# Kernel tuning notes

Hardware: AMD Instinct MI355X
Metric: run time of the kernel (lower is better)

The kernel has to match this reference:

```python
import jax, jax.numpy as jnp
import numpy as np

EPS = 1e-5


def _layernorm(x, w, b):
    mu = jnp.mean(x, axis=-1, keepdims=True)
    var = jnp.var(x, axis=-1, keepdims=True)
    return (x - mu) * jax.lax.rsqrt(var + EPS) * w + b


def setup_inputs() -> dict:
    key = jax.random.key(0)
    ks = jax.random.split(key, 5)
    B, I, H = 8192, 1024, 1024
    inp = {
        "input": jax.random.normal(ks[0], (B, I), dtype=jnp.float32),
        "hx": jax.random.normal(ks[1], (B, H), dtype=jnp.float32),
        "cx": jax.random.normal(ks[2], (B, H), dtype=jnp.float32),
        # parameters (torch initializes weights with randn; LN weight=1, bias=0)
        "weight_ih": jax.random.normal(ks[3], (4 * H, I), dtype=jnp.float32),
        "weight_hh": jax.random.normal(ks[4], (4 * H, H), dtype=jnp.float32),
        "ln_i_w": jnp.ones((4 * H,), jnp.float32),
        "ln_i_b": jnp.zeros((4 * H,), jnp.float32),
        "ln_h_w": jnp.ones((4 * H,), jnp.float32),
        "ln_h_b": jnp.zeros((4 * H,), jnp.float32),
        "ln_c_w": jnp.ones((H,), jnp.float32),
        "ln_c_b": jnp.zeros((H,), jnp.float32),
    }
    return inp


def reference(input, hx, cx, weight_ih, weight_hh,
              ln_i_w, ln_i_b, ln_h_w, ln_h_b, ln_c_w, ln_c_b):
    # gate pre-activations: [B, 4H]
    igates = _layernorm(input @ weight_ih.T, ln_i_w, ln_i_b)
    hgates = _layernorm(hx @ weight_hh.T, ln_h_w, ln_h_b)
    gates = igates + hgates
    ingate, forgetgate, cellgate, outgate = jnp.split(gates, 4, axis=-1)
    ingate = jax.nn.sigmoid(ingate)
    forgetgate = jax.nn.sigmoid(forgetgate)
    cellgate = jnp.tanh(cellgate)
    outgate = jax.nn.sigmoid(outgate)
    cy = _layernorm(forgetgate * cx + ingate * cellgate, ln_c_w, ln_c_b)
    hy = outgate * jnp.tanh(cy)  # activation=Tanh, dropout p=0 is identity
    return (hy, cy)
```

## Files before the change

### kernel.cpp

```cpp
#include <hip/hip_runtime.h>
#include <hip/hip_bf16.h>
#include <cstdint>
#include <cstddef>

typedef __bf16 bf16_t;
typedef bf16_t bf16x8 __attribute__((ext_vector_type(8)));
typedef bf16_t bf16x4v __attribute__((ext_vector_type(4)));
typedef float floatx4 __attribute__((ext_vector_type(4)));

static constexpr int B_ = 8192;
static constexpr int H_ = 1024;
static constexpr int G4 = 4096;
static constexpr int K_ = 1024;

__device__ inline void async_copy16(const bf16_t* g, bf16_t* l) {
  auto l3 = (__attribute__((address_space(3))) void*)(uint32_t)(uintptr_t)l;
  __builtin_amdgcn_global_load_lds(
      (__attribute__((address_space(1))) void*)(uintptr_t)g, l3, 16, 0, 0);
}

__global__ __launch_bounds__(256) void cast_f32_to_bf16(
    const float* __restrict__ src, bf16_t* __restrict__ dst, int n4) {
  int i = blockIdx.x * blockDim.x + threadIdx.x;
  if (i < n4) {
    const float4 v = ((const float4*)src)[i];
    bf16x4v o;
    o[0] = (bf16_t)v.x; o[1] = (bf16_t)v.y;
    o[2] = (bf16_t)v.z; o[3] = (bf16_t)v.w;
    ((bf16x4v*)dst)[i] = o;
  }
}

__global__ __launch_bounds__(256) void gemm_bt_dual(
    const bf16_t* __restrict__ A0, const bf16_t* __restrict__ A1,
    const bf16_t* __restrict__ W0, const bf16_t* __restrict__ W1,
    bf16_t* __restrict__ C0, bf16_t* __restrict__ C1) {
  constexpr int N = G4, K = K_;
  const bf16_t* A = blockIdx.z ? A1 : A0;
  const bf16_t* W = blockIdx.z ? W1 : W0;
  bf16_t*       C = blockIdx.z ? C1 : C0;

  __shared__ bf16_t As[128 * 32];
  __shared__ bf16_t Bs[128 * 32];

  const int tid  = threadIdx.x;
  const int lane = tid & 63;
  const int wid  = tid >> 6;
  const int wm   = wid >> 1, wn = wid & 1;
  const int lrow = lane & 15, quad = lane >> 4;

  const int m0 = blockIdx.y * 128;
  const int n0 = blockIdx.x * 128;

  const int L0 = tid;
  const int L1 = 256 + tid;
  const bf16_t* gA0 = A + (size_t)(m0 + (L0 >> 2)) * K + (L0 & 3) * 8;
  const bf16_t* gA1 = A + (size_t)(m0 + (L1 >> 2)) * K + (L1 & 3) * 8;
  const bf16_t* gB0 = W + (size_t)(n0 + (L0 >> 2)) * K + (L0 & 3) * 8;
  const bf16_t* gB1 = W + (size_t)(n0 + (L1 >> 2)) * K + (L1 & 3) * 8;
  bf16_t* lA0 = As + wid * 512;
  bf16_t* lA1 = As + 2048 + wid * 512;
  bf16_t* lB0 = Bs + wid * 512;
  bf16_t* lB1 = Bs + 2048 + wid * 512;

  floatx4 acc[4][4] = {};

  for (int k0 = 0; k0 < K; k0 += 32) {
    __syncthreads();
    async_copy16(gA0 + k0, lA0);
    async_copy16(gA1 + k0, lA1);
    async_copy16(gB0 + k0, lB0);
    async_copy16(gB1 + k0, lB1);
    __syncthreads();

    bf16x8 af[4], bfr[4];
#pragma unroll
    for (int i = 0; i < 4; ++i)
      af[i] = *(const bf16x8*)&As[(wm * 64 + i * 16 + lrow) * 32 + quad * 8];
#pragma unroll
    for (int j = 0; j < 4; ++j)
      bfr[j] = *(const bf16x8*)&Bs[(wn * 64 + j * 16 + lrow) * 32 + quad * 8];
#pragma unroll
    for (int i = 0; i < 4; ++i)
#pragma unroll
      for (int j = 0; j < 4; ++j)
        acc[i][j] = __builtin_amdgcn_mfma_f32_16x16x32_bf16(af[i], bfr[j],
                                                            acc[i][j], 0, 0, 0);
  }

#pragma unroll
  for (int i = 0; i < 4; ++i) {
    const int mbase = m0 + wm * 64 + i * 16 + quad * 4;
#pragma unroll
    for (int j = 0; j < 4; ++j) {
      const int n = n0 + wn * 64 + j * 16 + lrow;
#pragma unroll
      for (int r = 0; r < 4; ++r)
        C[(size_t)(mbase + r) * N + n] = (bf16_t)acc[i][j][r];
    }
  }
}

__device__ inline float sigmoid_f(float x) { return 1.0f / (1.0f + __expf(-x)); }
__device__ inline float tanh_f(float x) {
  float e = __expf(2.0f * x);
  return 1.0f - 2.0f / (e + 1.0f);
}
__device__ inline int swz(int n) { return n + (n >> 4); }

__global__ __launch_bounds__(256) void ln_lstm_epilogue(
    const bf16_t* __restrict__ IG, const bf16_t* __restrict__ HG,
    const float* __restrict__ cx,
    const float* __restrict__ wi, const float* __restrict__ bi,
    const float* __restrict__ wh, const float* __restrict__ bh,
    const float* __restrict__ wc, const float* __restrict__ bc,
    float* __restrict__ hy_out, float* __restrict__ cy_out) {
  const int b = blockIdx.x;
  const int tid = threadIdx.x;
  const int lane = tid & 63;
  const int wid = tid >> 6;

  __shared__ float gates[4096 + 256];
  __shared__ float red[4][4];

  const bf16_t* ig = IG + (size_t)b * 4096;
  const bf16_t* hg = HG + (size_t)b * 4096;

  float vi[16], vh[16];
  {
    bf16x8 a0 = *(const bf16x8*)(ig + tid * 16);
    bf16x8 a1 = *(const bf16x8*)(ig + tid * 16 + 8);
    bf16x8 c0 = *(const bf16x8*)(hg + tid * 16);
    bf16x8 c1 = *(const bf16x8*)(hg + tid * 16 + 8);
#pragma unroll
    for (int e = 0; e < 8; ++e) {
      vi[e] = (float)a0[e]; vi[8 + e] = (float)a1[e];
      vh[e] = (float)c0[e]; vh[8 + e] = (float)c1[e];
    }
  }
  float si = 0, qi = 0, sh = 0, qh = 0;
#pragma unroll
  for (int k = 0; k < 16; ++k) {
    si += vi[k]; qi = fmaf(vi[k], vi[k], qi);
    sh += vh[k]; qh = fmaf(vh[k], vh[k], qh);
  }
#pragma unroll
  for (int off = 32; off; off >>= 1) {
    si += __shfl_down(si, off); qi += __shfl_down(qi, off);
    sh += __shfl_down(sh, off); qh += __shfl_down(qh, off);
  }
  if (lane == 0) { red[wid][0] = si; red[wid][1] = qi; red[wid][2] = sh; red[wid][3] = qh; }
  __syncthreads();
  si = red[0][0] + red[1][0] + red[2][0] + red[3][0];
  qi = red[0][1] + red[1][1] + red[2][1] + red[3][1];
  sh = red[0][2] + red[1][2] + red[2][2] + red[3][2];
  qh = red[0][3] + red[1][3] + red[2][3] + red[3][3];

  const float invN = 1.0f / 4096.0f;
  const float mui = si * invN, muh = sh * invN;
  const float rsi = rsqrtf(fmaxf(qi * invN - mui * mui, 0.0f) + 1e-5f);
  const float rsh = rsqrtf(fmaxf(qh * invN - muh * muh, 0.0f) + 1e-5f);

#pragma unroll
  for (int k4 = 0; k4 < 4; ++k4) {
    const int nb = tid * 16 + k4 * 4;
    const float4 wiv = *(const float4*)(wi + nb);
    const float4 biv = *(const float4*)(bi + nb);
    const float4 whv = *(const float4*)(wh + nb);
    const float4 bhv = *(const float4*)(bh + nb);
    const float wia[4] = {wiv.x, wiv.y, wiv.z, wiv.w};
    const float bia[4] = {biv.x, biv.y, biv.z, biv.w};
    const float wha[4] = {whv.x, whv.y, whv.z, whv.w};
    const float bha[4] = {bhv.x, bhv.y, bhv.z, bhv.w};
#pragma unroll
    for (int j = 0; j < 4; ++j) {
      const int k = k4 * 4 + j;
      const float g = (vi[k] - mui) * rsi * wia[j] + bia[j] +
                      (vh[k] - muh) * rsh * wha[j] + bha[j];
      gates[swz(nb + j)] = g;
    }
  }
  __syncthreads();

  const float4 cx4 = *(const float4*)(cx + (size_t)b * 1024 + tid * 4);
  const float cxa[4] = {cx4.x, cx4.y, cx4.z, cx4.w};
  float cv[4], ov[4];
  float sc = 0, qc = 0;
#pragma unroll
  for (int j = 0; j < 4; ++j) {
    const int h = tid * 4 + j;
    const float in_g = sigmoid_f(gates[swz(h)]);
    const float fo_g = sigmoid_f(gates[swz(h + 1024)]);
    const float ce_g = tanh_f(gates[swz(h + 2048)]);
    ov[j] = sigmoid_f(gates[swz(h + 3072)]);
    const float c = fo_g * cxa[j] + in_g * ce_g;
    cv[j] = c;
    sc += c; qc = fmaf(c, c, qc);
  }
#pragma unroll
  for (int off = 32; off; off >>= 1) {
    sc += __shfl_down(sc, off); qc += __shfl_down(qc, off);
  }
  if (lane == 0) { red[wid][0] = sc; red[wid][1] = qc; }
  __syncthreads();
  sc = red[0][0] + red[1][0] + red[2][0] + red[3][0];
  qc = red[0][1] + red[1][1] + red[2][1] + red[3][1];
  const float invH = 1.0f / 1024.0f;
  const float muc = sc * invH;
  const float rsc = rsqrtf(fmaxf(qc * invH - muc * muc, 0.0f) + 1e-5f);

  const float4 wc4 = ((const float4*)wc)[tid];
  const float4 bc4 = ((const float4*)bc)[tid];
  const float wca[4] = {wc4.x, wc4.y, wc4.z, wc4.w};
  const float bca[4] = {bc4.x, bc4.y, bc4.z, bc4.w};
  float4 hyv, cyv;
  float cya[4], hya[4];
#pragma unroll
  for (int j = 0; j < 4; ++j) {
    const float cyn = (cv[j] - muc) * rsc * wca[j] + bca[j];
    cya[j] = cyn;
    hya[j] = ov[j] * tanh_f(cyn);
  }
  cyv.x = cya[0]; cyv.y = cya[1]; cyv.z = cya[2]; cyv.w = cya[3];
  hyv.x = hya[0]; hyv.y = hya[1]; hyv.z = hya[2]; hyv.w = hya[3];
  *(float4*)(cy_out + (size_t)b * 1024 + tid * 4) = cyv;
  *(float4*)(hy_out + (size_t)b * 1024 + tid * 4) = hyv;
}

extern "C" void kernel_launch(void* const* d_in, const int* in_sizes, int n_in,
                              void* d_out, int out_size, void* d_ws, size_t ws_size,
                              hipStream_t stream) {
  const float* input  = (const float*)d_in[0];
  const float* hx     = (const float*)d_in[1];
  const float* cx     = (const float*)d_in[2];
  const float* w_ih   = (const float*)d_in[3];
  const float* w_hh   = (const float*)d_in[4];
  const float* ln_i_w = (const float*)d_in[5];
  const float* ln_i_b = (const float*)d_in[6];
  const float* ln_h_w = (const float*)d_in[7];
  const float* ln_h_b = (const float*)d_in[8];
  const float* ln_c_w = (const float*)d_in[9];
  const float* ln_c_b = (const float*)d_in[10];

  float* out = (float*)d_out;
  float* hy = out;
  float* cy = out + (size_t)B_ * H_;

  bf16_t* Abf = (bf16_t*)d_ws;
  bf16_t* Hbf = Abf + (size_t)B_ * K_;
  bf16_t* Wib = Hbf + (size_t)B_ * K_;
  bf16_t* Whb = Wib + (size_t)G4 * K_;
  bf16_t* IG  = Whb + (size_t)G4 * K_;
  bf16_t* HG  = IG + (size_t)B_ * G4;

  const int T = 256;
  cast_f32_to_bf16<<<(B_ * K_ / 4 + T - 1) / T, T, 0, stream>>>(input, Abf, B_ * K_ / 4);
  cast_f32_to_bf16<<<(B_ * K_ / 4 + T - 1) / T, T, 0, stream>>>(hx, Hbf, B_ * K_ / 4);
  cast_f32_to_bf16<<<(G4 * K_ / 4 + T - 1) / T, T, 0, stream>>>(w_ih, Wib, G4 * K_ / 4);
  cast_f32_to_bf16<<<(G4 * K_ / 4 + T - 1) / T, T, 0, stream>>>(w_hh, Whb, G4 * K_ / 4);

  gemm_bt_dual<<<dim3(G4 / 128, B_ / 128, 2), 256, 0, stream>>>(Abf, Hbf, Wib, Whb, IG, HG);

  ln_lstm_epilogue<<<B_, 256, 0, stream>>>(IG, HG, cx, ln_i_w, ln_i_b,
                                           ln_h_w, ln_h_b, ln_c_w, ln_c_b, hy, cy);
}
```

Before: 428.4 us.

## Interleave gate rows in weights to drop LDS transpose in LSTM epilogue

Weight rows are permuted during the bf16 cast so the four gates for each hidden unit sit next to each other in the GEMM output columns. The epilogue then combines the gates in registers instead of staging 4096 floats through shared memory, which removes one barrier and the LDS traffic. The four cast launches are merged into two, with the input casts widened to 8 elements per thread. LayerNorm weights are now read strided per gate, and the permutation keeps per-row statistics unchanged.

Result: faster. 385.2 us (-10.1%).

```diff
diff --git a/kernel.cpp b/kernel.cpp
--- a/kernel.cpp
+++ b/kernel.cpp
@@ -19,16 +19,34 @@
       (__attribute__((address_space(1))) void*)(uintptr_t)g, l3, 16, 0, 0);
 }
 
-__global__ __launch_bounds__(256) void cast_f32_to_bf16(
-    const float* __restrict__ src, bf16_t* __restrict__ dst, int n4) {
-  int i = blockIdx.x * blockDim.x + threadIdx.x;
-  if (i < n4) {
-    const float4 v = ((const float4*)src)[i];
-    bf16x4v o;
-    o[0] = (bf16_t)v.x; o[1] = (bf16_t)v.y;
-    o[2] = (bf16_t)v.z; o[3] = (bf16_t)v.w;
-    ((bf16x4v*)dst)[i] = o;
-  }
+__global__ __launch_bounds__(256) void cast2_f32_bf16(
+    const float* __restrict__ a, const float* __restrict__ b,
+    bf16_t* __restrict__ oa, bf16_t* __restrict__ ob, int n8each) {
+  int gid = blockIdx.x * blockDim.x + threadIdx.x;
+  const float* src; bf16_t* dst; int idx;
+  if (gid < n8each) { src = a; dst = oa; idx = gid; }
+  else              { src = b; dst = ob; idx = gid - n8each; }
+  const float4 v0 = ((const float4*)src)[idx * 2];
+  const float4 v1 = ((const float4*)src)[idx * 2 + 1];
+  bf16x8 o;
+  o[0] = (bf16_t)v0.x; o[1] = (bf16_t)v0.y; o[2] = (bf16_t)v0.z; o[3] = (bf16_t)v0.w;
+  o[4] = (bf16_t)v1.x; o[5] = (bf16_t)v1.y; o[6] = (bf16_t)v1.z; o[7] = (bf16_t)v1.w;
+  ((bf16x8*)dst)[idx] = o;
+}
+
+__global__ __launch_bounds__(256) void cast_w_perm(
+    const float* __restrict__ wih, const float* __restrict__ whh,
+    bf16_t* __restrict__ oih, bf16_t* __restrict__ ohh) {
+  const int rp = blockIdx.x & 4095;
+  const float* src = (blockIdx.x < 4096) ? wih : whh;
+  bf16_t*      dst = (blockIdx.x < 4096) ? oih : ohh;
+  const int h = rp >> 2, g = rp & 3;
+  const int rin = g * 1024 + h;
+  const int c = threadIdx.x * 4;
+  const float4 v = *(const float4*)(src + (size_t)rin * K_ + c);
+  bf16x4v o;
+  o[0] = (bf16_t)v.x; o[1] = (bf16_t)v.y; o[2] = (bf16_t)v.z; o[3] = (bf16_t)v.w;
+  *(bf16x4v*)(dst + (size_t)rp * K_ + c) = o;
 }
 
 __global__ __launch_bounds__(256) void gemm_bt_dual(
@@ -106,7 +124,6 @@
   float e = __expf(2.0f * x);
   return 1.0f - 2.0f / (e + 1.0f);
 }
-__device__ inline int swz(int n) { return n + (n >> 4); }
 
 __global__ __launch_bounds__(256) void ln_lstm_epilogue(
     const bf16_t* __restrict__ IG, const bf16_t* __restrict__ HG,
@@ -116,27 +133,24 @@
     const float* __restrict__ wc, const float* __restrict__ bc,
     float* __restrict__ hy_out, float* __restrict__ cy_out) {
   const int b = blockIdx.x;
-  const int tid = threadIdx.x;
-  const int lane = tid & 63;
-  const int wid = tid >> 6;
-
-  __shared__ float gates[4096 + 256];
-  __shared__ float red[4][4];
-
-  const bf16_t* ig = IG + (size_t)b * 4096;
-  const bf16_t* hg = HG + (size_t)b * 4096;
+  const int t = threadIdx.x;
+  const int lane = t & 63;
+  const int wid = t >> 6;
+
+  __shared__ float red1[4][4];
+  __shared__ float red2[4][2];
+
+  const bf16x8 ig0 = *(const bf16x8*)(IG + (size_t)b * 4096 + t * 16);
+  const bf16x8 ig1 = *(const bf16x8*)(IG + (size_t)b * 4096 + t * 16 + 8);
+  const bf16x8 hg0 = *(const bf16x8*)(HG + (size_t)b * 4096 + t * 16);
+  const bf16x8 hg1 = *(const bf16x8*)(HG + (size_t)b * 4096 + t * 16 + 8);
+  const float4 cx4 = *(const float4*)(cx + (size_t)b * 1024 + t * 4);
 
   float vi[16], vh[16];
-  {
-    bf16x8 a0 = *(const bf16x8*)(ig + tid * 16);
-    bf16x8 a1 = *(const bf16x8*)(ig + tid * 16 + 8);
-    bf16x8 c0 = *(const bf16x8*)(hg + tid * 16);
-    bf16x8 c1 = *(const bf16x8*)(hg + tid * 16 + 8);
-#pragma unroll
-    for (int e = 0; e < 8; ++e) {
-      vi[e] = (float)a0[e]; vi[8 + e] = (float)a1[e];
-      vh[e] = (float)c0[e]; vh[8 + e] = (float)c1[e];
-    }
+#pragma unroll
+  for (int e = 0; e < 8; ++e) {
+    vi[e] = (float)ig0[e]; vi[8 + e] = (float)ig1[e];
+    vh[e] = (float)hg0[e]; vh[8 + e] = (float)hg1[e];
   }
   float si = 0, qi = 0, sh = 0, qh = 0;
 #pragma unroll
@@ -149,50 +163,51 @@
     si += __shfl_down(si, off); qi += __shfl_down(qi, off);
     sh += __shfl_down(sh, off); qh += __shfl_down(qh, off);
   }
-  if (lane == 0) { red[wid][0] = si; red[wid][1] = qi; red[wid][2] = sh; red[wid][3] = qh; }
+  if (lane == 0) { red1[wid][0] = si; red1[wid][1] = qi; red1[wid][2] = sh; red1[wid][3] = qh; }
   __syncthreads();
-  si = red[0][0] + red[1][0] + red[2][0] + red[3][0];
-  qi = red[0][1] + red[1][1] + red[2][1] + red[3][1];
-  sh = red[0][2] + red[1][2] + red[2][2] + red[3][2];
-  qh = red[0][3] + red[1][3] + red[2][3] + red[3][3];
+  si = red1[0][0] + red1[1][0] + red1[2][0] + red1[3][0];
+  qi = red1[0][1] + red1[1][1] + red1[2][1] + red1[3][1];
+  sh = red1[0][2] + red1[1][2] + red1[2][2] + red1[3][2];
+  qh = red1[0][3] + red1[1][3] + red1[2][3] + red1[3][3];
 
   const float invN = 1.0f / 4096.0f;
   const float mui = si * invN, muh = sh * invN;
   const float rsi = rsqrtf(fmaxf(qi * invN - mui * mui, 0.0f) + 1e-5f);
   const float rsh = rsqrtf(fmaxf(qh * invN - muh * muh, 0.0f) + 1e-5f);
 
-#pragma unroll
-  for (int k4 = 0; k4 < 4; ++k4) {
-    const int nb = tid * 16 + k4 * 4;
-    const float4 wiv = *(const float4*)(wi + nb);
-    const float4 biv = *(const float4*)(bi + nb);
-    const float4 whv = *(const float4*)(wh + nb);
-    const float4 bhv = *(const float4*)(bh + nb);
-    const float wia[4] = {wiv.x, wiv.y, wiv.z, wiv.w};
-    const float bia[4] = {biv.x, biv.y, biv.z, biv.w};
-    const float wha[4] = {whv.x, whv.y, whv.z, whv.w};
-    const float bha[4] = {bhv.x, bhv.y, bhv.z, bhv.w};
-#pragma unroll
-    for (int j = 0; j < 4; ++j) {
-      const int k = k4 * 4 + j;
-      const float g = (vi[k] - mui) * rsi * wia[j] + bia[j] +
-                      (vh[k] - muh) * rsh * wha[j] + bha[j];
-      gates[swz(nb + j)] = g;
-    }
-  }
-  __syncthreads();
-
-  const float4 cx4 = *(const float4*)(cx + (size_t)b * 1024 + tid * 4);
+  float4 wig[4], big[4], whg[4], bhg[4];
+#pragma unroll
+  for (int g = 0; g < 4; ++g) {
+    wig[g] = *(const float4*)(wi + g * 1024 + t * 4);
+    big[g] = *(const float4*)(bi + g * 1024 + t * 4);
+    whg[g] = *(const float4*)(wh + g * 1024 + t * 4);
+    bhg[g] = *(const float4*)(bh + g * 1024 + t * 4);
+  }
+
   const float cxa[4] = {cx4.x, cx4.y, cx4.z, cx4.w};
   float cv[4], ov[4];
   float sc = 0, qc = 0;
 #pragma unroll
   for (int j = 0; j < 4; ++j) {
-    const int h = tid * 4 + j;
-    const float in_g = sigmoid_f(gates[swz(h)]);
-    const float fo_g = sigmoid_f(gates[swz(h + 1024)]);
-    const float ce_g = tanh_f(gates[swz(h + 2048)]);
-    ov[j] = sigmoid_f(gates[swz(h + 3072)]);
+    const float wg[4] = {((const float*)&wig[0])[j], ((const float*)&wig[1])[j],
+                         ((const float*)&wig[2])[j], ((const float*)&wig[3])[j]};
+    const float bg[4] = {((const float*)&big[0])[j], ((const float*)&big[1])[j],
+                         ((const float*)&big[2])[j], ((const float*)&big[3])[j]};
+    const float wg2[4] = {((const float*)&whg[0])[j], ((const float*)&whg[1])[j],
+                          ((const float*)&whg[2])[j], ((const float*)&whg[3])[j]};
+    const float bg2[4] = {((const float*)&bhg[0])[j], ((const float*)&bhg[1])[j],
+                          ((const float*)&bhg[2])[j], ((const float*)&bhg[3])[j]};
+    float G[4];
+#pragma unroll
+    for (int g = 0; g < 4; ++g) {
+      const int e = j * 4 + g;
+      G[g] = (vi[e] - mui) * rsi * wg[g] + bg[g] +
+             (vh[e] - muh) * rsh * wg2[g] + bg2[g];
+    }
+    const float in_g = sigmoid_f(G[0]);
+    const float fo_g = sigmoid_f(G[1]);
+    const float ce_g = tanh_f(G[2]);
+    ov[j] = sigmoid_f(G[3]);
     const float c = fo_g * cxa[j] + in_g * ce_g;
     cv[j] = c;
     sc += c; qc = fmaf(c, c, qc);
@@ -201,30 +216,27 @@
   for (int off = 32; off; off >>= 1) {
     sc += __shfl_down(sc, off); qc += __shfl_down(qc, off);
   }
-  if (lane == 0) { red[wid][0] = sc; red[wid][1] = qc; }
+  if (lane == 0) { red2[wid][0] = sc; red2[wid][1] = qc; }
   __syncthreads();
-  sc = red[0][0] + red[1][0] + red[2][0] + red[3][0];
-  qc = red[0][1] + red[1][1] + red[2][1] + red[3][1];
+  sc = red2[0][0] + red2[1][0] + red2[2][0] + red2[3][0];
+  qc = red2[0][1] + red2[1][1] + red2[2][1] + red2[3][1];
   const float invH = 1.0f / 1024.0f;
   const float muc = sc * invH;
   const float rsc = rsqrtf(fmaxf(qc * invH - muc * muc, 0.0f) + 1e-5f);
 
-  const float4 wc4 = ((const float4*)wc)[tid];
-  const float4 bc4 = ((const float4*)bc)[tid];
+  const float4 wc4 = ((const float4*)wc)[t];
+  const float4 bc4 = ((const float4*)bc)[t];
   const float wca[4] = {wc4.x, wc4.y, wc4.z, wc4.w};
   const float bca[4] = {bc4.x, bc4.y, bc4.z, bc4.w};
   float4 hyv, cyv;
-  float cya[4], hya[4];
 #pragma unroll
   for (int j = 0; j < 4; ++j) {
     const float cyn = (cv[j] - muc) * rsc * wca[j] + bca[j];
-    cya[j] = cyn;
-    hya[j] = ov[j] * tanh_f(cyn);
-  }
-  cyv.x = cya[0]; cyv.y = cya[1]; cyv.z = cya[2]; cyv.w = cya[3];
-  hyv.x = hya[0]; hyv.y = hya[1]; hyv.z = hya[2]; hyv.w = hya[3];
-  *(float4*)(cy_out + (size_t)b * 1024 + tid * 4) = cyv;
-  *(float4*)(hy_out + (size_t)b * 1024 + tid * 4) = hyv;
+    ((float*)&cyv)[j] = cyn;
+    ((float*)&hyv)[j] = ov[j] * tanh_f(cyn);
+  }
+  *(float4*)(cy_out + (size_t)b * 1024 + t * 4) = cyv;
+  *(float4*)(hy_out + (size_t)b * 1024 + t * 4) = hyv;
 }
 
 extern "C" void kernel_launch(void* const* d_in, const int* in_sizes, int n_in,
@@ -253,11 +265,9 @@
   bf16_t* IG  = Whb + (size_t)G4 * K_;
   bf16_t* HG  = IG + (size_t)B_ * G4;
 
-  const int T = 256;
-  cast_f32_to_bf16<<<(B_ * K_ / 4 + T - 1) / T, T, 0, stream>>>(input, Abf, B_ * K_ / 4);
-  cast_f32_to_bf16<<<(B_ * K_ / 4 + T - 1) / T, T, 0, stream>>>(hx, Hbf, B_ * K_ / 4);
-  cast_f32_to_bf16<<<(G4 * K_ / 4 + T - 1) / T, T, 0, stream>>>(w_ih, Wib, G4 * K_ / 4);
-  cast_f32_to_bf16<<<(G4 * K_ / 4 + T - 1) / T, T, 0, stream>>>(w_hh, Whb, G4 * K_ / 4);
+  const int n8 = B_ * K_ / 8;
+  cast2_f32_bf16<<<(2 * n8) / 256, 256, 0, stream>>>(input, hx, Abf, Hbf, n8);
+  cast_w_perm<<<2 * G4, 256, 0, stream>>>(w_ih, w_hh, Wib, Whb);
 
   gemm_bt_dual<<<dim3(G4 / 128, B_ / 128, 2), 256, 0, stream>>>(Abf, Hbf, Wib, Whb, IG, HG);
 
```
